# Performance work log

Hardware: AMD Instinct MI355X
Metric: run time of the kernel (lower is better)

## Reference

```python
import jax, jax.numpy as jnp
import numpy as np

N, E, C, L, G, O = 100000, 1600000, 128, 7, 2, 40
BETA = 0.9
HEADS, HC = 1, 128  # heads=1, head_channels=hidden_channels=128


def setup_inputs() -> dict:
    key = jax.random.key(0)
    ks = jax.random.split(key, 16)
    s = 0.05  # ~ torch Linear init std for fan_in=128
    inp = {
        'x': jax.random.normal(ks[0], (N, C), jnp.float32),
        'edge_index': jax.random.randint(ks[1], (2, E), 0, N, jnp.int64),
        'Wh': jax.random.normal(ks[2], (L, C, C)) * s,
        'bh': jax.random.normal(ks[3], (L, C)) * s,
        'Wg': jax.random.normal(ks[4], (L, C, C)) * s,
        'bg': jax.random.normal(ks[5], (L, C)) * s,
        'Wl': jax.random.normal(ks[6], (L, C, C)) * s,
        'bl': jax.random.normal(ks[7], (L, C)) * s,
        'ln_g': jnp.ones((L, C)), 'ln_b': jnp.zeros((L, C)),
        'bn_g': jnp.ones((L, C)), 'bn_b': jnp.zeros((L, C)),
        'bn_rm': jnp.zeros((L, C)), 'bn_rv': jnp.ones((L, C)),
        'gWh': jax.random.normal(ks[8], (G, C, C)) * s,
        'gbh': jax.random.normal(ks[9], (G, C)) * s,
        'gWk': jax.random.normal(ks[10], (G, C, C)) * s,
        'gWv': jax.random.normal(ks[11], (G, C, C)) * s,
        'gln_g': jnp.ones((G, C)), 'gln_b': jnp.zeros((G, C)),
        'gWo': jax.random.normal(ks[12], (G, C, C)) * s,
        'gbo': jax.random.normal(ks[13], (G, C)) * s,
        'f_ln_g': jnp.ones((C,)), 'f_ln_b': jnp.zeros((C,)),
        'Wp': jax.random.normal(ks[14], (O, C)) * s,
        'bp': jax.random.normal(ks[15], (O,)) * s,
    }
    return inp


def _layer_norm(x, g, b, eps=1e-5):
    mu = jnp.mean(x, axis=-1, keepdims=True)
    var = jnp.mean((x - mu) ** 2, axis=-1, keepdims=True)
    return (x - mu) * jax.lax.rsqrt(var + eps) * g + b


def reference(x, edge_index, Wh, bh, Wg, bg, Wl, bl, ln_g, ln_b,
              bn_g, bn_b, bn_rm, bn_rv, gWh, gbh, gWk, gWv,
              gln_g, gln_b, gWo, gbo, f_ln_g, f_ln_b, Wp, bp):
    n = x.shape[0]
    src, dst = edge_index[0], edge_index[1]
    # gcn_norm with add_self_loops=True: deg over destination incl. self loop
    deg = jnp.zeros((n,), x.dtype).at[dst].add(1.0) + 1.0
    dinv = jax.lax.rsqrt(deg)
    enorm = (dinv[src] * dinv[dst])[:, None]   # [E,1]
    selfw = (dinv * dinv)[:, None]             # [N,1] self-loop weight

    x_local = jnp.zeros_like(x @ Wh[0].T)
    for i in range(L):
        h = jax.nn.relu(x @ Wh[i].T + bh[i])
        xw = x @ Wg[i].T                                  # GCN lin (bias separate)
        agg = jax.ops.segment_sum(xw[src] * enorm, dst, num_segments=n)
        conv = agg + xw * selfw + bg[i]
        x = conv + x @ Wl[i].T + bl[i]
        # BatchNorm1d in eval mode (running stats)
        x = (x - bn_rm[i]) * jax.lax.rsqrt(bn_rv[i] + 1e-5) * bn_g[i] + bn_b[i]
        x = jax.nn.relu(x)
        x = (1.0 - BETA) * _layer_norm(h * x, ln_g[i], ln_b[i]) + BETA * x
        x_local = x_local + x

    # global linear attention (PolynormerAttention, qk_shared=True, qkv_bias=False)
    xg = _layer_norm(x_local, f_ln_g, f_ln_b)
    for j in range(G):
        h = xg @ gWh[j].T + gbh[j]
        k = jax.nn.sigmoid(xg @ gWk[j].T).reshape(n, HEADS, HC)
        q = k
        v = (xg @ gWv[j].T).reshape(n, HEADS, HC)
        kv = jnp.einsum('ndh,ndm->dhm', k, v)            # [heads,hc,hc]
        num = jnp.einsum('ndh,dhm->ndm', q, kv)          # [N,heads,hc]
        k_sum = jnp.sum(k, axis=0)                       # [heads,hc]
        den = jnp.einsum('ndh,dh->nd', q, k_sum)[..., None]
        attn = (num / (den + 1e-6)).reshape(n, HEADS * HC)
        xg = _layer_norm(attn, gln_g[j], gln_b[j]) * (h + BETA)
        xg = jax.nn.relu(xg @ gWo[j].T + gbo[j])

    return xg @ Wp.T + bp
```

## Files before the change

kernel.cpp:

```cpp
#include <hip/hip_runtime.h>

typedef unsigned short u16;
typedef unsigned int u32;
typedef __attribute__((ext_vector_type(8))) short short8;
typedef __attribute__((ext_vector_type(8))) unsigned short ushort8v;
typedef __attribute__((ext_vector_type(4))) float f32x4;

#define CDIM 128

__device__ __forceinline__ float b2f(u16 u){ return __uint_as_float(((unsigned)u)<<16); }
__device__ __forceinline__ u16 f2b(float f){
  unsigned x = __float_as_uint(f);
  unsigned r = (x + 0x7fffu + ((x>>16)&1u)) >> 16;
  return (u16)r;
}
__device__ __forceinline__ float wsum64(float v){
  #pragma unroll
  for(int d=1; d<64; d<<=1) v += __shfl_xor(v, d, 64);
  return v;
}
__device__ __forceinline__ float wsum16(float v){
  v += __shfl_xor(v, 1, 64);
  v += __shfl_xor(v, 2, 64);
  v += __shfl_xor(v, 4, 64);
  v += __shfl_xor(v, 8, 64);
  return v;
}

__global__ void k_probe(const u32* __restrict__ x, const u32* __restrict__ ei, int* __restrict__ flags){
  __shared__ int s_bf, s_nz;
  if(threadIdx.x == 0){ s_bf = 0; s_nz = 0; }
  __syncthreads();
  int c_bf = 0, c_nz = 0;
  for(int i = threadIdx.x; i < 4096; i += 256){
    u32 w = x[i];
    u32 e = (w >> 7) & 0xFFu;
    if(e >= 100u && e <= 140u) c_bf++;
    if(ei[2*i + 1] != 0u) c_nz++;
  }
  atomicAdd(&s_bf, c_bf);
  atomicAdd(&s_nz, c_nz);
  __syncthreads();
  if(threadIdx.x == 0){
    flags[0] = (s_bf < 2048) ? 1 : 0;
    flags[1] = (s_nz < 8) ? 1 : 0;
  }
}

__global__ void k_cvt_x(const void* __restrict__ src, u16* __restrict__ dst, int n,
                        const int* __restrict__ flags){
  int i = (blockIdx.x*256 + threadIdx.x)*8;
  if(i + 7 >= n) return;
  if(flags[0]){
    const float* s = (const float*)src + i;
    float4 a = *(const float4*)s;
    float4 b = *(const float4*)(s + 4);
    ushort8v o;
    o[0]=f2b(a.x); o[1]=f2b(a.y); o[2]=f2b(a.z); o[3]=f2b(a.w);
    o[4]=f2b(b.x); o[5]=f2b(b.y); o[6]=f2b(b.z); o[7]=f2b(b.w);
    *(ushort8v*)(dst + i) = o;
  } else {
    *(ushort8v*)(dst + i) = *(const ushort8v*)((const u16*)src + i);
  }
}

struct CvtArgs {
  const void* src[24];
  u16* dst[24];
  int n[24];
};

__global__ void k_cvt_params(CvtArgs a, const int* __restrict__ flags){
  int seg = blockIdx.y;
  int i = blockIdx.x*256 + threadIdx.x;
  int n = a.n[seg];
  if(i >= n) return;
  if(flags[0]) a.dst[seg][i] = f2b(((const float*)a.src[seg])[i]);
  else         a.dst[seg][i] = ((const u16*)a.src[seg])[i];
}

__global__ void k_cvt_ei_count(const int* __restrict__ src, int* __restrict__ dst, int E,
                               const int* __restrict__ flags, u32* __restrict__ cnt){
  int i = blockIdx.x*256 + threadIdx.x;
  if(i >= 2*E) return;
  int v = flags[1] ? src[2*i] : src[i];
  dst[i] = v;
  if(i >= E) atomicAdd(&cnt[v], 1u);
}

__global__ __launch_bounds__(256) void k_scan1(const u32* __restrict__ cnt, int n, u32* __restrict__ bsum){
  const int lane = threadIdx.x & 63;
  const int wv = threadIdx.x >> 6;
  int i = blockIdx.x*256 + threadIdx.x;
  u32 v = (i < n) ? cnt[i] : 0u;
  #pragma unroll
  for(int d=1; d<64; d<<=1) v += (u32)__shfl_xor((int)v, d, 64);
  __shared__ u32 ws[4];
  if(lane == 0) ws[wv] = v;
  __syncthreads();
  if(threadIdx.x == 0) bsum[blockIdx.x] = ws[0] + ws[1] + ws[2] + ws[3];
}

__global__ __launch_bounds__(1024) void k_scan2(const u32* __restrict__ bsum, int nb, u32* __restrict__ bpre){
  __shared__ u32 s[1024];
  int t = threadIdx.x;
  u32 v = (t < nb) ? bsum[t] : 0u;
  s[t] = v;
  __syncthreads();
  for(int d=1; d<1024; d<<=1){
    u32 y = (t >= d) ? s[t-d] : 0u;
    __syncthreads();
    s[t] += y;
    __syncthreads();
  }
  if(t < nb) bpre[t] = s[t] - v;
}

__global__ __launch_bounds__(256) void k_scan3(const u32* __restrict__ cnt, int n,
                                               const u32* __restrict__ bpre,
                                               u32* __restrict__ rowstart, u32* __restrict__ cursor,
                                               float* __restrict__ dinv){
  const int lane = threadIdx.x & 63;
  const int wv = threadIdx.x >> 6;
  int i = blockIdx.x*256 + threadIdx.x;
  u32 v = (i < n) ? cnt[i] : 0u;
  u32 x = v;
  #pragma unroll
  for(int d=1; d<64; d<<=1){
    u32 y = (u32)__shfl_up((int)x, d, 64);
    if(lane >= d) x += y;
  }
  __shared__ u32 ws[4];
  if(lane == 63) ws[wv] = x;
  __syncthreads();
  u32 woff = 0;
  #pragma unroll
  for(int w=0; w<4; w++) if(w < wv) woff += ws[w];
  u32 incl = x + woff;
  u32 rs = bpre[blockIdx.x] + incl - v;
  if(i < n){
    rowstart[i] = rs;
    cursor[i] = rs;
    dinv[i] = rsqrtf((float)(v + 1u));
    if(i == n-1) rowstart[n] = rs + v;
  }
}

__global__ __launch_bounds__(256) void k_scatter8(
  const int* __restrict__ ei, int E, int Nn, int nsl,
  u32* __restrict__ cursor, const float* __restrict__ dinv, int2* __restrict__ colw)
{
  const int r = blockIdx.x & 7;
  const int slice = blockIdx.x >> 3;
  const int q = (Nn + 7) >> 3;
  const int lo = r*q;
  const int hi = (lo + q < Nn) ? lo + q : Nn;
  const int chunk = (E + nsl - 1) / nsl;
  int e0 = slice*chunk;
  int e1 = e0 + chunk; if(e1 > E) e1 = E;
  for(int e = e0 + threadIdx.x; e < e1; e += 256){
    int d = ei[E + e];
    if(d >= lo && d < hi){
      int s = ei[e];
      u32 p = atomicAdd(&cursor[d], 1u);
      colw[p] = make_int2(s, __float_as_int(dinv[s]));
    }
  }
}

__global__ __launch_bounds__(256) void k_gemm3(
  const u16* __restrict__ A, int M,
  const u16* __restrict__ W0, const u16* __restrict__ bs0, int op0, u16* __restrict__ O0,
  const u16* __restrict__ W1, const u16* __restrict__ bs1, int op1, u16* __restrict__ O1,
  const u16* __restrict__ W2, const u16* __restrict__ bs2, int op2, u16* __restrict__ O2)
{
  const int lane = threadIdx.x & 63;
  const int wv = threadIdx.x >> 6;
  const int l16 = lane & 15, quad = lane >> 4;
  const long nbase = (long)blockIdx.x*128 + wv*32;

  short8 xf[2][4];
  #pragma unroll
  for(int nt=0; nt<2; nt++){
    long r = nbase + nt*16 + l16; if(r >= M) r = M-1;
    const u16* ap = A + r*CDIM + quad*8;
    #pragma unroll
    for(int kt=0; kt<4; kt++)
      xf[nt][kt] = *(const short8*)(ap + kt*32);
  }

  const u16* Ws[3] = {W0, W1, W2};
  const u16* Bs[3] = {bs0, bs1, bs2};
  u16* Os[3] = {O0, O1, O2};
  const int ops[3] = {op0, op1, op2};

  for(int w=0; w<3; w++){
    const u16* Wm = Ws[w];
    if(!Wm) break;
    const int op = ops[w];
    u16* Op = Os[w];
    const u16* bp = Bs[w];

    #pragma unroll
    for(int ct=0; ct<8; ct++){
      f32x4 acc0 = {0.f,0.f,0.f,0.f}, acc1 = {0.f,0.f,0.f,0.f};
      const u16* wp = Wm + (ct*16 + l16)*CDIM + quad*8;
      #pragma unroll
      for(int kt=0; kt<4; kt++){
        short8 wf = *(const short8*)(wp + kt*32);
        acc0 = __builtin_amdgcn_mfma_f32_16x16x32_bf16(wf, xf[0][kt], acc0, 0, 0, 0);
        acc1 = __builtin_amdgcn_mfma_f32_16x16x32_bf16(wf, xf[1][kt], acc1, 0, 0, 0);
      }
      float bv[4] = {0.f,0.f,0.f,0.f};
      if(bp){
        ushort4 bq = *(const ushort4*)(bp + ct*16 + quad*4);
        bv[0]=b2f(bq.x); bv[1]=b2f(bq.y); bv[2]=b2f(bq.z); bv[3]=b2f(bq.w);
      }
      #pragma unroll
      for(int nt=0; nt<2; nt++){
        long node = nbase + nt*16 + l16;
        if(node < M){
          f32x4 a = nt ? acc1 : acc0;
          u16 o[4];
          #pragma unroll
          for(int g=0; g<4; g++){
            float v = a[g] + bv[g];
            if(op == 1) v = fmaxf(v, 0.f);
            else if(op == 2) v = 1.f/(1.f + __expf(-v));
            o[g] = f2b(v);
          }
          u32 p0 = (u32)o[0] | ((u32)o[1] << 16);
          u32 p1 = (u32)o[2] | ((u32)o[3] << 16);
          *(uint2*)(Op + (size_t)node*CDIM + ct*16 + quad*4) = make_uint2(p0, p1);
        }
      }
    }
  }
}

__global__ __launch_bounds__(256) void k_layer_epi(
  const u16* __restrict__ xw, const u16* __restrict__ h, const u16* __restrict__ xl,
  const int2* __restrict__ colw, const u32* __restrict__ rowstart, const float* __restrict__ dinv,
  const u16* __restrict__ bg, const u16* __restrict__ bng, const u16* __restrict__ bnb,
  const u16* __restrict__ bnrm, const u16* __restrict__ bnrv,
  const u16* __restrict__ lng, const u16* __restrict__ lnb,
  const u16* __restrict__ flng, const u16* __restrict__ flnb,
  float* __restrict__ xlocal, u16* __restrict__ xout, int n, int first, int final)
{
  const int lane = threadIdx.x & 63;
  const int node = blockIdx.x*4 + (threadIdx.x >> 6);
  if(node >= n) return;
  const int c0 = lane*2;
  u32 j0 = rowstart[node], j1 = rowstart[node+1];
  float a0 = 0.f, a1 = 0.f;
  for(u32 base = j0; base < j1; base += 64){
    int avail = (int)(j1 - base);
    int cnt = avail < 64 ? avail : 64;
    int2 pw = make_int2(0, 0);
    if(lane < cnt) pw = colw[base + lane];
    int cntp = (cnt + 7) & ~7;
    for(int t = 0; t < cntp; t += 8){
      int s[8]; float w[8]; ushort2 v[8];
      #pragma unroll
      for(int k2=0;k2<8;k2++){
        s[k2] = __shfl(pw.x, t+k2, 64);
        w[k2] = __int_as_float(__shfl(pw.y, t+k2, 64));
      }
      #pragma unroll
      for(int k2=0;k2<8;k2++) v[k2] = *(const ushort2*)(xw + (size_t)s[k2]*CDIM + c0);
      #pragma unroll
      for(int k2=0;k2<8;k2++){
        a0 = fmaf(w[k2], b2f(v[k2].x), a0);
        a1 = fmaf(w[k2], b2f(v[k2].y), a1);
      }
    }
  }
  float dn = dinv[node], sw = dn*dn;
  size_t base = (size_t)node*CDIM + c0;
  ushort2 xwv = *(const ushort2*)(xw + base);
  ushort2 xlv = *(const ushort2*)(xl + base);
  ushort2 hv  = *(const ushort2*)(h  + base);
  float x10 = a0*dn + b2f(xwv.x)*sw + b2f(bg[c0])   + b2f(xlv.x);
  float x11 = a1*dn + b2f(xwv.y)*sw + b2f(bg[c0+1]) + b2f(xlv.y);
  float s0 = rsqrtf(b2f(bnrv[c0])   + 1e-5f) * b2f(bng[c0]);
  float s1 = rsqrtf(b2f(bnrv[c0+1]) + 1e-5f) * b2f(bng[c0+1]);
  float x20 = (x10 - b2f(bnrm[c0]))*s0   + b2f(bnb[c0]);
  float x21 = (x11 - b2f(bnrm[c0+1]))*s1 + b2f(bnb[c0+1]);
  float x30 = fmaxf(x20, 0.f);
  float x31 = fmaxf(x21, 0.f);
  float t0 = b2f(hv.x)*x30, t1 = b2f(hv.y)*x31;
  float mu = wsum64(t0 + t1) * (1.f/128.f);
  float d0 = t0 - mu, d1 = t1 - mu;
  float var = wsum64(d0*d0 + d1*d1) * (1.f/128.f);
  float inv = rsqrtf(var + 1e-5f);
  float y0 = d0*inv*b2f(lng[c0])   + b2f(lnb[c0]);
  float y1 = d1*inv*b2f(lng[c0+1]) + b2f(lnb[c0+1]);
  float xn0 = 0.1f*y0 + 0.9f*x30;
  float xn1 = 0.1f*y1 + 0.9f*x31;
  float2 xl2;
  if(first){
    xl2.x = xn0; xl2.y = xn1;
  } else {
    xl2 = *(float2*)(xlocal + base);
    xl2.x += xn0; xl2.y += xn1;
  }
  if(!final){
    *(float2*)(xlocal + base) = xl2;
    ushort2 o; o.x = f2b(xn0); o.y = f2b(xn1);
    *(ushort2*)(xout + base) = o;
  } else {
    float mu2 = wsum64(xl2.x + xl2.y) * (1.f/128.f);
    float e0 = xl2.x - mu2, e1 = xl2.y - mu2;
    float var2 = wsum64(e0*e0 + e1*e1) * (1.f/128.f);
    float inv2 = rsqrtf(var2 + 1e-5f);
    ushort2 o;
    o.x = f2b(e0*inv2*b2f(flng[c0])   + b2f(flnb[c0]));
    o.y = f2b(e1*inv2*b2f(flng[c0+1]) + b2f(flnb[c0+1]));
    *(ushort2*)(xout + base) = o;
  }
}

__global__ __launch_bounds__(256) void k_kv(
  const u16* __restrict__ kk, const u16* __restrict__ vv, int n, int npb,
  float* __restrict__ part)
{
  __shared__ float sk[8][128];
  __shared__ float sv[8][128];
  const int tid = threadIdx.x;
  const int tr = tid >> 4, tc = tid & 15;
  float acc[8][8];
  #pragma unroll
  for(int i=0;i<8;i++){
    #pragma unroll
    for(int j=0;j<8;j++) acc[i][j] = 0.f;
  }
  float ks[8];
  #pragma unroll
  for(int i=0;i<8;i++) ks[i] = 0.f;
  int start = blockIdx.x * npb;
  int end = start + npb; if(end > n) end = n;
  const int lr = tid >> 5;
  const int lc = (tid & 31) * 4;
  for(int g0 = start; g0 < end; g0 += 8){
    int cnt = end - g0; if(cnt > 8) cnt = 8;
    __syncthreads();
    if(lr < cnt){
      ushort4 kq = *(const ushort4*)(kk + (size_t)(g0+lr)*CDIM + lc);
      ushort4 vq = *(const ushort4*)(vv + (size_t)(g0+lr)*CDIM + lc);
      sk[lr][lc] = b2f(kq.x); sk[lr][lc+1] = b2f(kq.y); sk[lr][lc+2] = b2f(kq.z); sk[lr][lc+3] = b2f(kq.w);
      sv[lr][lc] = b2f(vq.x); sv[lr][lc+1] = b2f(vq.y); sv[lr][lc+2] = b2f(vq.z); sv[lr][lc+3] = b2f(vq.w);
    }
    __syncthreads();
    for(int r=0; r<cnt; r++){
      float4 ka = *(const float4*)&sk[r][tr*8];
      float4 kb = *(const float4*)&sk[r][tr*8+4];
      float4 va = *(const float4*)&sv[r][tc*8];
      float4 vb = *(const float4*)&sv[r][tc*8+4];
      float kr[8] = {ka.x,ka.y,ka.z,ka.w,kb.x,kb.y,kb.z,kb.w};
      float vr[8] = {va.x,va.y,va.z,va.w,vb.x,vb.y,vb.z,vb.w};
      #pragma unroll
      for(int i=0;i<8;i++){
        #pragma unroll
        for(int j=0;j<8;j++) acc[i][j] = fmaf(kr[i], vr[j], acc[i][j]);
      }
      if(tc == 0){
        #pragma unroll
        for(int i=0;i<8;i++) ks[i] += kr[i];
      }
    }
  }
  float* p = part + (size_t)blockIdx.x * 16512;
  #pragma unroll
  for(int i=0;i<8;i++){
    #pragma unroll
    for(int j=0;j<8;j++)
      p[(size_t)(tc*8+j)*CDIM + tr*8 + i] = acc[i][j];
  }
  if(tc == 0){
    #pragma unroll
    for(int i=0;i<8;i++) p[16384 + tr*8 + i] = ks[i];
  }
}

__global__ void k_kvred(const float* __restrict__ part, int nb, u16* __restrict__ Bext){
  int i = blockIdx.x*256 + threadIdx.x;
  if(i >= 144*128) return;
  float s = 0.f;
  if(i < 16512){
    #pragma unroll 8
    for(int b=0;b<nb;b++) s += part[(size_t)b*16512 + i];
  }
  Bext[i] = f2b(s);
}

__global__ __launch_bounds__(256) void k_attn(
  const u16* __restrict__ q, const u16* __restrict__ Bext, const u16* __restrict__ hg,
  const u16* __restrict__ g, const u16* __restrict__ b,
  u16* __restrict__ out, int M)
{
  const int lane = threadIdx.x & 63;
  const int wv = threadIdx.x >> 6;
  const int l16 = lane & 15, quad = lane >> 4;
  const long rbase = (long)blockIdx.x*128 + wv*32;

  short8 af[2][4];
  #pragma unroll
  for(int rt=0; rt<2; rt++){
    long r = rbase + rt*16 + l16; if(r >= M) r = M-1;
    const u16* ap = q + r*CDIM + quad*8;
    #pragma unroll
    for(int kt=0; kt<4; kt++)
      af[rt][kt] = *(const short8*)(ap + kt*32);
  }
  f32x4 acc[2][9];
  f32x4 zero = {0.f,0.f,0.f,0.f};
  #pragma unroll
  for(int rt=0; rt<2; rt++){
    #pragma unroll
    for(int ct=0; ct<9; ct++) acc[rt][ct] = zero;
  }
  #pragma unroll
  for(int ct=0; ct<9; ct++){
    const u16* wp = Bext + (ct*16 + l16)*CDIM + quad*8;
    #pragma unroll
    for(int kt=0; kt<4; kt++){
      short8 bf = *(const short8*)(wp + kt*32);
      acc[0][ct] = __builtin_amdgcn_mfma_f32_16x16x32_bf16(af[0][kt], bf, acc[0][ct], 0, 0, 0);
      acc[1][ct] = __builtin_amdgcn_mfma_f32_16x16x32_bf16(af[1][kt], bf, acc[1][ct], 0, 0, 0);
    }
  }
  #pragma unroll
  for(int rt=0; rt<2; rt++){
    float rden[4];
    #pragma unroll
    for(int gi=0; gi<4; gi++){
      float dv = __shfl(acc[rt][8][gi], lane & 48, 64);
      rden[gi] = 1.f/(dv + 1e-6f);
    }
    #pragma unroll
    for(int gi=0; gi<4; gi++){
      float sum = 0.f;
      #pragma unroll
      for(int ct=0; ct<8; ct++) sum += acc[rt][ct][gi]*rden[gi];
      float mu = wsum16(sum) * (1.f/128.f);
      float vs = 0.f;
      #pragma unroll
      for(int ct=0; ct<8; ct++){ float d = acc[rt][ct][gi]*rden[gi] - mu; vs = fmaf(d, d, vs); }
      float inv = rsqrtf(wsum16(vs)*(1.f/128.f) + 1e-5f);
      long r = rbase + rt*16 + quad*4 + gi;
      if(r < M){
        #pragma unroll
        for(int ct=0; ct<8; ct++){
          int col = ct*16 + l16;
          float y = (acc[rt][ct][gi]*rden[gi] - mu)*inv*b2f(g[col]) + b2f(b[col]);
          float hvv = b2f(hg[(size_t)r*CDIM + col]);
          out[(size_t)r*CDIM + col] = f2b(y*(hvv + 0.9f));
        }
      }
    }
  }
}

__global__ __launch_bounds__(256) void k_gout(
  const u16* __restrict__ A, const u16* __restrict__ W, const u16* __restrict__ bs,
  void* __restrict__ outv, int M, const int* __restrict__ flags)
{
  const int lane = threadIdx.x & 63;
  const int wv = threadIdx.x >> 6;
  const int l16 = lane & 15, quad = lane >> 4;
  const long rbase = (long)blockIdx.x*128 + wv*32;
  const int f32m = flags[0];
  short8 af[2][4];
  #pragma unroll
  for(int rt=0; rt<2; rt++){
    long r = rbase + rt*16 + l16; if(r >= M) r = M-1;
    const u16* ap = A + r*CDIM + quad*8;
    #pragma unroll
    for(int kt=0; kt<4; kt++)
      af[rt][kt] = *(const short8*)(ap + kt*32);
  }
  f32x4 acc[2][3];
  f32x4 zero = {0.f,0.f,0.f,0.f};
  #pragma unroll
  for(int rt=0; rt<2; rt++){
    #pragma unroll
    for(int ct=0; ct<3; ct++) acc[rt][ct] = zero;
  }
  #pragma unroll
  for(int ct=0; ct<3; ct++){
    int row = ct*16 + l16; if(row > 39) row = 39;
    const u16* wp = W + row*CDIM + quad*8;
    #pragma unroll
    for(int kt=0; kt<4; kt++){
      short8 bf = *(const short8*)(wp + kt*32);
      acc[0][ct] = __builtin_amdgcn_mfma_f32_16x16x32_bf16(af[0][kt], bf, acc[0][ct], 0, 0, 0);
      acc[1][ct] = __builtin_amdgcn_mfma_f32_16x16x32_bf16(af[1][kt], bf, acc[1][ct], 0, 0, 0);
    }
  }
  #pragma unroll
  for(int ct=0; ct<3; ct++){
    int col = ct*16 + l16;
    if(col < 40){
      float bias = b2f(bs[col]);
      #pragma unroll
      for(int rt=0; rt<2; rt++){
        #pragma unroll
        for(int gi=0; gi<4; gi++){
          long r = rbase + rt*16 + quad*4 + gi;
          if(r < M){
            float v = acc[rt][ct][gi] + bias;
            if(f32m) ((float*)outv)[r*40 + col] = v;
            else     ((u16*)outv)[r*40 + col] = f2b(v);
          }
        }
      }
    }
  }
}

extern "C" void kernel_launch(void* const* d_in, const int* in_sizes, int n_in,
                              void* d_out, int out_size, void* d_ws, size_t ws_size,
                              hipStream_t stream)
{
  (void)n_in;
  const int C = CDIM;
  const int Nn = in_sizes[0] / C;
  const int E  = in_sizes[1] / 2;

  char* ws = (char*)d_ws;
  size_t off = 0;
  auto alloc = [&](size_t bytes) -> char* {
    char* p = ws + off;
    off = (off + bytes + 255) & ~(size_t)255;
    return p;
  };
  u16*   x_cur  = (u16*)  alloc((size_t)Nn*C*2);
  float* xlocal = (float*)alloc((size_t)Nn*C*4);
  u16*   hb     = (u16*)  alloc((size_t)Nn*C*2);
  u16*   xwb    = (u16*)  alloc((size_t)Nn*C*2);
  u16*   xlb    = (u16*)  alloc((size_t)Nn*C*2);
  float* dinv   = (float*)alloc((size_t)Nn*4);
  u32*   cnt    = (u32*)  alloc((size_t)Nn*4);
  u32*   rowst  = (u32*)  alloc((size_t)(Nn+1)*4);
  u32*   cursor = (u32*)  alloc((size_t)Nn*4);
  int2*  colw   = (int2*) alloc((size_t)E*8);
  u16*   Bext   = (u16*)  alloc((size_t)144*128*2);
  int*   flags  = (int*)  alloc(256);
  u32*   bsum   = (u32*)  alloc(1024*4);
  u32*   bpre   = (u32*)  alloc(1024*4);
  size_t ptot = 0;
  for(int k=2;k<26;k++) ptot += (size_t)in_sizes[k];
  u16* pbuf = (u16*)alloc(ptot*2);

  if(off > ws_size){
    hipMemsetAsync(d_out, 0, (size_t)out_size*2, stream);
    return;
  }

  const u16* pp[26];
  {
    size_t po = 0;
    for(int k=2;k<26;k++){ pp[k] = pbuf + po; po += (size_t)in_sizes[k]; }
  }
  const u16* cWh  = pp[2];  const u16* cbh  = pp[3];
  const u16* cWg  = pp[4];  const u16* cbg  = pp[5];
  const u16* cWl  = pp[6];  const u16* cbl  = pp[7];
  const u16* clng = pp[8];  const u16* clnb = pp[9];
  const u16* cbng = pp[10]; const u16* cbnb = pp[11];
  const u16* cbnrm= pp[12]; const u16* cbnrv= pp[13];
  const u16* cgWh = pp[14]; const u16* cgbh = pp[15];
  const u16* cgWk = pp[16]; const u16* cgWv = pp[17];
  const u16* cglng= pp[18]; const u16* cglnb= pp[19];
  const u16* cgWo = pp[20]; const u16* cgbo = pp[21];
  const u16* cflng= pp[22]; const u16* cflnb= pp[23];
  const u16* cWp  = pp[24]; const u16* cbp  = pp[25];

  u16* xb  = (u16*)xlocal;
  int* eib = (int*)((char*)xlocal + (size_t)Nn*C*2);
  u16* xg  = x_cur;
  float* kvpart = xlocal;

  const int NB_KV = 512;
  const int npb = (Nn + NB_KV - 1) / NB_KV;
  const int gblk = (Nn + 127) / 128;
  const int nodeblk = (Nn + 3) / 4;
  const int nscan = (Nn + 255) / 256;
  const int NSL = 512;

  k_probe<<<1, 256, 0, stream>>>((const u32*)d_in[0], (const u32*)d_in[1], flags);
  hipMemsetAsync(cnt, 0, (size_t)Nn*4, stream);
  k_cvt_ei_count<<<(2*E + 255)/256, 256, 0, stream>>>((const int*)d_in[1], eib, E, flags, cnt);
  k_cvt_x<<<(Nn*C/8 + 255)/256, 256, 0, stream>>>(d_in[0], xb, Nn*C, flags);
  {
    CvtArgs a;
    int maxn = 0;
    for(int k=2;k<26;k++){
      a.src[k-2] = d_in[k];
      a.dst[k-2] = (u16*)pp[k];
      a.n[k-2]   = in_sizes[k];
      if(in_sizes[k] > maxn) maxn = in_sizes[k];
    }
    dim3 g((maxn + 255)/256, 24);
    k_cvt_params<<<g, 256, 0, stream>>>(a, flags);
  }

  k_scan1<<<nscan, 256, 0, stream>>>(cnt, Nn, bsum);
  k_scan2<<<1, 1024, 0, stream>>>(bsum, nscan, bpre);
  k_scan3<<<nscan, 256, 0, stream>>>(cnt, Nn, bpre, rowst, cursor, dinv);
  k_scatter8<<<NSL*8, 256, 0, stream>>>(eib, E, Nn, NSL, cursor, dinv, colw);

  const u16* xa = xb;
  for(int i=0; i<7; i++){
    k_gemm3<<<gblk, 256, 0, stream>>>(xa, Nn,
        cWh + (size_t)i*C*C, cbh + (size_t)i*C, 1, hb,
        cWg + (size_t)i*C*C, (const u16*)nullptr, 0, xwb,
        cWl + (size_t)i*C*C, cbl + (size_t)i*C, 0, xlb);
    k_layer_epi<<<nodeblk, 256, 0, stream>>>(xwb, hb, xlb, colw, rowst, dinv,
        cbg + (size_t)i*C, cbng + (size_t)i*C, cbnb + (size_t)i*C,
        cbnrm + (size_t)i*C, cbnrv + (size_t)i*C,
        clng + (size_t)i*C, clnb + (size_t)i*C,
        cflng, cflnb,
        xlocal, x_cur, Nn, (i==0) ? 1 : 0, (i==6) ? 1 : 0);
    xa = x_cur;
  }

  for(int j=0; j<2; j++){
    k_gemm3<<<gblk, 256, 0, stream>>>(xg, Nn,
        cgWh + (size_t)j*C*C, cgbh + (size_t)j*C, 0, hb,
        cgWk + (size_t)j*C*C, (const u16*)nullptr, 2, xwb,
        cgWv + (size_t)j*C*C, (const u16*)nullptr, 0, xlb);
    k_kv   <<<NB_KV, 256, 0, stream>>>(xwb, xlb, Nn, npb, kvpart);
    k_kvred<<<(144*128 + 255)/256, 256, 0, stream>>>(kvpart, NB_KV, Bext);
    k_attn <<<gblk, 256, 0, stream>>>(xwb, Bext, hb, cglng + (size_t)j*C, cglnb + (size_t)j*C, xlb, Nn);
    k_gemm3<<<gblk, 256, 0, stream>>>(xlb, Nn,
        cgWo + (size_t)j*C*C, cgbo + (size_t)j*C, 1, xg,
        (const u16*)nullptr, (const u16*)nullptr, 0, (u16*)nullptr,
        (const u16*)nullptr, (const u16*)nullptr, 0, (u16*)nullptr);
  }

  k_gout<<<gblk, 256, 0, stream>>>(xg, cWp, cbp, d_out, Nn, flags);
}
```

Measured before the change: 1.738 ms.

## Split fused GEMM over weight matrices via grid.y and vectorize edge gather

The three-weight GEMM kernel now assigns each weight matrix to a separate grid-y slice, so every block computes one output instead of looping over all three. This triples the block count and parallelism, at the cost of reloading the A tile once per weight. The layer epilogue's neighbour aggregation now has each quarter-wave gather a different edge with 16-byte row loads (8 channels per lane) instead of 4-byte loads. The partial sums are combined with cross-quad shuffles and redistributed through shared memory. Out-of-range waves are clamped rather than returning early so the new __syncthreads is safe.

```diff
diff --git a/kernel.cpp b/kernel.cpp
--- a/kernel.cpp
+++ b/kernel.cpp
@@ -179,60 +179,57 @@
   const int l16 = lane & 15, quad = lane >> 4;
   const long nbase = (long)blockIdx.x*128 + wv*32;
 
-  short8 xf[2][4];
-  #pragma unroll
-  for(int nt=0; nt<2; nt++){
-    long r = nbase + nt*16 + l16; if(r >= M) r = M-1;
-    const u16* ap = A + r*CDIM + quad*8;
-    #pragma unroll
-    for(int kt=0; kt<4; kt++)
-      xf[nt][kt] = *(const short8*)(ap + kt*32);
-  }
-
   const u16* Ws[3] = {W0, W1, W2};
   const u16* Bs[3] = {bs0, bs1, bs2};
   u16* Os[3] = {O0, O1, O2};
   const int ops[3] = {op0, op1, op2};
-
-  for(int w=0; w<3; w++){
-    const u16* Wm = Ws[w];
-    if(!Wm) break;
-    const int op = ops[w];
-    u16* Op = Os[w];
-    const u16* bp = Bs[w];
-
-    #pragma unroll
-    for(int ct=0; ct<8; ct++){
-      f32x4 acc0 = {0.f,0.f,0.f,0.f}, acc1 = {0.f,0.f,0.f,0.f};
-      const u16* wp = Wm + (ct*16 + l16)*CDIM + quad*8;
-      #pragma unroll
-      for(int kt=0; kt<4; kt++){
-        short8 wf = *(const short8*)(wp + kt*32);
-        acc0 = __builtin_amdgcn_mfma_f32_16x16x32_bf16(wf, xf[0][kt], acc0, 0, 0, 0);
-        acc1 = __builtin_amdgcn_mfma_f32_16x16x32_bf16(wf, xf[1][kt], acc1, 0, 0, 0);
-      }
-      float bv[4] = {0.f,0.f,0.f,0.f};
-      if(bp){
-        ushort4 bq = *(const ushort4*)(bp + ct*16 + quad*4);
-        bv[0]=b2f(bq.x); bv[1]=b2f(bq.y); bv[2]=b2f(bq.z); bv[3]=b2f(bq.w);
-      }
-      #pragma unroll
-      for(int nt=0; nt<2; nt++){
-        long node = nbase + nt*16 + l16;
-        if(node < M){
-          f32x4 a = nt ? acc1 : acc0;
-          u16 o[4];
-          #pragma unroll
-          for(int g=0; g<4; g++){
-            float v = a[g] + bv[g];
-            if(op == 1) v = fmaxf(v, 0.f);
-            else if(op == 2) v = 1.f/(1.f + __expf(-v));
-            o[g] = f2b(v);
-          }
-          u32 p0 = (u32)o[0] | ((u32)o[1] << 16);
-          u32 p1 = (u32)o[2] | ((u32)o[3] << 16);
-          *(uint2*)(Op + (size_t)node*CDIM + ct*16 + quad*4) = make_uint2(p0, p1);
+  const int w = blockIdx.y;
+  const u16* Wm = Ws[w];
+  const int op = ops[w];
+  u16* Op = Os[w];
+  const u16* bp = Bs[w];
+
+  short8 xf[2][4];
+  #pragma unroll
+  for(int nt=0; nt<2; nt++){
+    long r = nbase + nt*16 + l16; if(r >= M) r = M-1;
+    const u16* ap = A + r*CDIM + quad*8;
+    #pragma unroll
+    for(int kt=0; kt<4; kt++)
+      xf[nt][kt] = *(const short8*)(ap + kt*32);
+  }
+
+  #pragma unroll
+  for(int ct=0; ct<8; ct++){
+    f32x4 acc0 = {0.f,0.f,0.f,0.f}, acc1 = {0.f,0.f,0.f,0.f};
+    const u16* wp = Wm + (ct*16 + l16)*CDIM + quad*8;
+    #pragma unroll
+    for(int kt=0; kt<4; kt++){
+      short8 wf = *(const short8*)(wp + kt*32);
+      acc0 = __builtin_amdgcn_mfma_f32_16x16x32_bf16(wf, xf[0][kt], acc0, 0, 0, 0);
+      acc1 = __builtin_amdgcn_mfma_f32_16x16x32_bf16(wf, xf[1][kt], acc1, 0, 0, 0);
+    }
+    float bv[4] = {0.f,0.f,0.f,0.f};
+    if(bp){
+      ushort4 bq = *(const ushort4*)(bp + ct*16 + quad*4);
+      bv[0]=b2f(bq.x); bv[1]=b2f(bq.y); bv[2]=b2f(bq.z); bv[3]=b2f(bq.w);
+    }
+    #pragma unroll
+    for(int nt=0; nt<2; nt++){
+      long node = nbase + nt*16 + l16;
+      if(node < M){
+        f32x4 a = nt ? acc1 : acc0;
+        u16 o[4];
+        #pragma unroll
+        for(int g=0; g<4; g++){
+          float v = a[g] + bv[g];
+          if(op == 1) v = fmaxf(v, 0.f);
+          else if(op == 2) v = 1.f/(1.f + __expf(-v));
+          o[g] = f2b(v);
         }
+        u32 p0 = (u32)o[0] | ((u32)o[1] << 16);
+        u32 p1 = (u32)o[2] | ((u32)o[3] << 16);
+        *(uint2*)(Op + (size_t)node*CDIM + ct*16 + quad*4) = make_uint2(p0, p1);
       }
     }
   }
@@ -247,34 +244,56 @@
   const u16* __restrict__ flng, const u16* __restrict__ flnb,
   float* __restrict__ xlocal, u16* __restrict__ xout, int n, int first, int final)
 {
+  __shared__ float redis[4][128];
   const int lane = threadIdx.x & 63;
-  const int node = blockIdx.x*4 + (threadIdx.x >> 6);
-  if(node >= n) return;
-  const int c0 = lane*2;
+  const int quad = lane >> 4;
+  const int l16 = lane & 15;
+  const int wv = threadIdx.x >> 6;
+  int node = blockIdx.x*4 + wv;
+  const int valid = (node < n);
+  if(!valid) node = n - 1;
+  const int cg = l16*8;
   u32 j0 = rowstart[node], j1 = rowstart[node+1];
-  float a0 = 0.f, a1 = 0.f;
+  float a[8];
+  #pragma unroll
+  for(int g=0; g<8; g++) a[g] = 0.f;
+
   for(u32 base = j0; base < j1; base += 64){
     int avail = (int)(j1 - base);
     int cnt = avail < 64 ? avail : 64;
     int2 pw = make_int2(0, 0);
     if(lane < cnt) pw = colw[base + lane];
-    int cntp = (cnt + 7) & ~7;
-    for(int t = 0; t < cntp; t += 8){
-      int s[8]; float w[8]; ushort2 v[8];
+    int cntp = (cnt + 15) & ~15;
+    for(int t = 0; t < cntp; t += 16){
+      int s[4]; float w[4]; ushort8v v[4];
       #pragma unroll
-      for(int k2=0;k2<8;k2++){
-        s[k2] = __shfl(pw.x, t+k2, 64);
-        w[k2] = __int_as_float(__shfl(pw.y, t+k2, 64));
+      for(int u=0; u<4; u++){
+        s[u] = __shfl(pw.x, t + u*4 + quad, 64);
+        w[u] = __int_as_float(__shfl(pw.y, t + u*4 + quad, 64));
       }
       #pragma unroll
-      for(int k2=0;k2<8;k2++) v[k2] = *(const ushort2*)(xw + (size_t)s[k2]*CDIM + c0);
+      for(int u=0; u<4; u++) v[u] = *(const ushort8v*)(xw + (size_t)s[u]*CDIM + cg);
       #pragma unroll
-      for(int k2=0;k2<8;k2++){
-        a0 = fmaf(w[k2], b2f(v[k2].x), a0);
-        a1 = fmaf(w[k2], b2f(v[k2].y), a1);
+      for(int u=0; u<4; u++){
+        #pragma unroll
+        for(int g=0; g<8; g++) a[g] = fmaf(w[u], b2f(v[u][g]), a[g]);
       }
     }
   }
+  #pragma unroll
+  for(int g=0; g<8; g++){
+    a[g] += __shfl_xor(a[g], 16, 64);
+    a[g] += __shfl_xor(a[g], 32, 64);
+  }
+  if(quad == 0){
+    *(float4*)&redis[wv][cg]     = make_float4(a[0],a[1],a[2],a[3]);
+    *(float4*)&redis[wv][cg + 4] = make_float4(a[4],a[5],a[6],a[7]);
+  }
+  __syncthreads();
+  const int c0 = lane*2;
+  float2 av = *(float2*)&redis[wv][c0];
+  float a0 = av.x, a1 = av.y;
+
   float dn = dinv[node], sw = dn*dn;
   size_t base = (size_t)node*CDIM + c0;
   ushort2 xwv = *(const ushort2*)(xw + base);
@@ -305,18 +324,22 @@
     xl2.x += xn0; xl2.y += xn1;
   }
   if(!final){
-    *(float2*)(xlocal + base) = xl2;
-    ushort2 o; o.x = f2b(xn0); o.y = f2b(xn1);
-    *(ushort2*)(xout + base) = o;
+    if(valid){
+      *(float2*)(xlocal + base) = xl2;
+      ushort2 o; o.x = f2b(xn0); o.y = f2b(xn1);
+      *(ushort2*)(xout + base) = o;
+    }
   } else {
     float mu2 = wsum64(xl2.x + xl2.y) * (1.f/128.f);
     float e0 = xl2.x - mu2, e1 = xl2.y - mu2;
     float var2 = wsum64(e0*e0 + e1*e1) * (1.f/128.f);
     float inv2 = rsqrtf(var2 + 1e-5f);
-    ushort2 o;
-    o.x = f2b(e0*inv2*b2f(flng[c0])   + b2f(flnb[c0]));
-    o.y = f2b(e1*inv2*b2f(flng[c0+1]) + b2f(flnb[c0+1]));
-    *(ushort2*)(xout + base) = o;
+    if(valid){
+      ushort2 o;
+      o.x = f2b(e0*inv2*b2f(flng[c0])   + b2f(flnb[c0]));
+      o.y = f2b(e1*inv2*b2f(flng[c0+1]) + b2f(flnb[c0+1]));
+      *(ushort2*)(xout + base) = o;
+    }
   }
 }
 
@@ -611,7 +634,7 @@
 
   const u16* xa = xb;
   for(int i=0; i<7; i++){
-    k_gemm3<<<gblk, 256, 0, stream>>>(xa, Nn,
+    k_gemm3<<<dim3(gblk,3), 256, 0, stream>>>(xa, Nn,
         cWh + (size_t)i*C*C, cbh + (size_t)i*C, 1, hb,
         cWg + (size_t)i*C*C, (const u16*)nullptr, 0, xwb,
         cWl + (size_t)i*C*C, cbl + (size_t)i*C, 0, xlb);
@@ -625,14 +648,14 @@
   }
 
   for(int j=0; j<2; j++){
-    k_gemm3<<<gblk, 256, 0, stream>>>(xg, Nn,
+    k_gemm3<<<dim3(gblk,3), 256, 0, stream>>>(xg, Nn,
         cgWh + (size_t)j*C*C, cgbh + (size_t)j*C, 0, hb,
         cgWk + (size_t)j*C*C, (const u16*)nullptr, 2, xwb,
         cgWv + (size_t)j*C*C, (const u16*)nullptr, 0, xlb);
     k_kv   <<<NB_KV, 256, 0, stream>>>(xwb, xlb, Nn, npb, kvpart);
     k_kvred<<<(144*128 + 255)/256, 256, 0, stream>>>(kvpart, NB_KV, Bext);
     k_attn <<<gblk, 256, 0, stream>>>(xwb, Bext, hb, cglng + (size_t)j*C, cglnb + (size_t)j*C, xlb, Nn);
-    k_gemm3<<<gblk, 256, 0, stream>>>(xlb, Nn,
+    k_gemm3<<<dim3(gblk,1), 256, 0, stream>>>(xlb, Nn,
         cgWo + (size_t)j*C*C, cgbo + (size_t)j*C, 1, xg,
         (const u16*)nullptr, (const u16*)nullptr, 0, (u16*)nullptr,
         (const u16*)nullptr, (const u16*)nullptr, 0, (u16*)nullptr);
```

Result: no change. 1.710 ms (-1.6%).
